# Kernel optimization log

Measured on AMD Instinct MI355X. Metric: run time of the kernel, lower is better.

Reference implementation:

```python
import jax, jax.numpy as jnp
import numpy as np

B, C, H, W = 4, 256, 64, 64
CQ = C // 8


def setup_inputs() -> dict:
    key = jax.random.key(0)
    ks = jax.random.split(key, 8)
    s = 0.02
    return {
        "x": jax.random.normal(ks[0], (B, C, H, W), dtype=jnp.float32),
        "Wq": jax.random.normal(ks[1], (CQ, C), dtype=jnp.float32) * s,
        "bq": jax.random.normal(ks[2], (CQ,), dtype=jnp.float32) * s,
        "Wk": jax.random.normal(ks[3], (CQ, C), dtype=jnp.float32) * s,
        "bk": jax.random.normal(ks[4], (CQ,), dtype=jnp.float32) * s,
        "Wv": jax.random.normal(ks[5], (C, C), dtype=jnp.float32) * s,
        "bv": jax.random.normal(ks[6], (C,), dtype=jnp.float32) * s,
        "gamma": jax.random.normal(ks[7], (1,), dtype=jnp.float32) * s,
    }


def reference(x, Wq, bq, Wk, bk, Wv, bv, gamma):
    b, c, h, w = x.shape
    n = h * w
    xf = x.reshape(b, c, n)  # [B,C,N]; 1x1 conv == channel matmul
    q = jnp.einsum("oc,bcn->bno", Wq, xf) + bq  # [B,N,CQ]
    k = jnp.einsum("oc,bcn->bon", Wk, xf) + bk[:, None]  # [B,CQ,N]
    v = jnp.einsum("oc,bcn->bno", Wv, xf) + bv  # [B,N,C]
    attn = jnp.einsum("bnd,bdm->bnm", q, k)  # [B,N,N], unscaled
    attn = jax.nn.softmax(attn, axis=1)  # non-standard axis (over rows)
    out = jnp.einsum("bnm,bmc->bnc", attn, v)  # [B,N,C]
    out = out.transpose(0, 2, 1).reshape(b, c, h, w)
    return gamma * out + x
```

## Files before the change

kernel.cpp:

```cpp
#include <hip/hip_runtime.h>

#define B_ 4
#define C_ 256
#define N_ 4096
#define LOG2E 1.44269504088896340736f

typedef __attribute__((ext_vector_type(8))) short bf16x8;
typedef __attribute__((ext_vector_type(4))) float f32x4;

static __device__ __forceinline__ unsigned short f2bf(float f) {
    unsigned u = __builtin_bit_cast(unsigned, f);
    u += 0x7fffu + ((u >> 16) & 1u);
    return (unsigned short)(u >> 16);
}

static __device__ __forceinline__ float fexp2(float x) {
#if __has_builtin(__builtin_amdgcn_exp2f)
    return __builtin_amdgcn_exp2f(x);
#else
    return exp2f(x);
#endif
}

#define AS1 __attribute__((address_space(1)))
#define AS3 __attribute__((address_space(3)))
static __device__ __forceinline__ void gload_lds16(const void* g, void* l) {
    __builtin_amdgcn_global_load_lds((const AS1 unsigned*)g, (AS3 unsigned*)l, 16, 0, 0);
}

__global__ void k0_wprep(const float* __restrict__ Wq, const float* __restrict__ Wk,
                         const float* __restrict__ Wv, float* __restrict__ WqkT,
                         float* __restrict__ WvT) {
    int t = blockIdx.x * 256 + threadIdx.x;
    if (t < 256 * 64) {
        int c = t >> 6, o = t & 63;
        WqkT[t] = (o < 32) ? Wq[o * C_ + c] * LOG2E : Wk[(o - 32) * C_ + c];
    }
    int t2 = t - 256 * 64;
    if (t2 >= 0 && t2 < 256 * 256) {
        int cp = t2 >> 8, c = t2 & 255;
        WvT[t2] = Wv[c * C_ + cp];
    }
}

__global__ __launch_bounds__(256) void k1_qk(const float* __restrict__ x,
        const float* __restrict__ WqkT, const float* __restrict__ bq,
        const float* __restrict__ bk, unsigned short* __restrict__ qb,
        unsigned short* __restrict__ ktb) {
    __shared__ float red[4][64][33];
    int b = blockIdx.z, isk = blockIdx.y;
    int l = threadIdx.x & 63, v = threadIdx.x >> 6;
    int n = blockIdx.x * 64 + l;
    float acc[32];
#pragma unroll
    for (int o = 0; o < 32; ++o) acc[o] = 0.0f;
    const float* xp = x + (size_t)b * C_ * N_ + n;
    const float* wbase = WqkT + (isk ? 32 : 0);
#pragma unroll 4
    for (int c = 64 * v; c < 64 * v + 64; ++c) {
        float xv = xp[(size_t)c * N_];
        const float* wr = wbase + c * 64;
#pragma unroll
        for (int o = 0; o < 32; ++o) acc[o] += wr[o] * xv;
    }
#pragma unroll
    for (int o = 0; o < 32; ++o) red[v][l][o] = acc[o];
    __syncthreads();
    int nl = threadIdx.x & 63, ob = (threadIdx.x >> 6) * 8;
    const float* bias = isk ? bk : bq;
    float bs = isk ? 1.0f : LOG2E;
    unsigned pk[4];
#pragma unroll
    for (int i = 0; i < 4; ++i) {
        int o0 = ob + 2 * i, o1 = ob + 2 * i + 1;
        float v0 = red[0][nl][o0] + red[1][nl][o0] + red[2][nl][o0] + red[3][nl][o0] + bias[o0] * bs;
        float v1 = red[0][nl][o1] + red[1][nl][o1] + red[2][nl][o1] + red[3][nl][o1] + bias[o1] * bs;
        pk[i] = (unsigned)f2bf(v0) | ((unsigned)f2bf(v1) << 16);
    }
    unsigned short* dst = (isk ? ktb : qb) + ((size_t)b * N_ + blockIdx.x * 64 + nl) * 32 + ob;
    *(uint4*)dst = make_uint4(pk[0], pk[1], pk[2], pk[3]);
}

__global__ __launch_bounds__(512) void k2_stats(const unsigned short* __restrict__ qb,
        const unsigned short* __restrict__ ktb, float* __restrict__ Wcol) {
    __shared__ float red[64][33];
    int b = blockIdx.y;
    int m0 = blockIdx.x * 64;
    int lane = threadIdx.x & 63, w = threadIdx.x >> 6;
    int r16 = lane & 15, g = lane >> 4;
    const unsigned short* kb = ktb + ((size_t)b * N_ + m0 + r16) * 32 + 8 * g;
    bf16x8 kf0 = *(const bf16x8*)(kb);
    bf16x8 kf1 = *(const bf16x8*)(kb + 16 * 32);
    bf16x8 kf2 = *(const bf16x8*)(kb + 32 * 32);
    bf16x8 kf3 = *(const bf16x8*)(kb + 48 * 32);
    float z0 = 0, z1 = 0, z2 = 0, z3 = 0;
    const unsigned short* qbase = qb + ((size_t)b * N_ + w * 512 + r16) * 32 + 8 * g;
#pragma unroll 2
    for (int n0 = 0; n0 < 512; n0 += 16) {
        bf16x8 qf = *(const bf16x8*)(qbase + (size_t)n0 * 32);
        f32x4 d0 = __builtin_amdgcn_mfma_f32_16x16x32_bf16(qf, kf0, (f32x4){0, 0, 0, 0}, 0, 0, 0);
        f32x4 d1 = __builtin_amdgcn_mfma_f32_16x16x32_bf16(qf, kf1, (f32x4){0, 0, 0, 0}, 0, 0, 0);
        f32x4 d2 = __builtin_amdgcn_mfma_f32_16x16x32_bf16(qf, kf2, (f32x4){0, 0, 0, 0}, 0, 0, 0);
        f32x4 d3 = __builtin_amdgcn_mfma_f32_16x16x32_bf16(qf, kf3, (f32x4){0, 0, 0, 0}, 0, 0, 0);
        z0 += fexp2(d0[0]) + fexp2(d0[1]) + fexp2(d0[2]) + fexp2(d0[3]);
        z1 += fexp2(d1[0]) + fexp2(d1[1]) + fexp2(d1[2]) + fexp2(d1[3]);
        z2 += fexp2(d2[0]) + fexp2(d2[1]) + fexp2(d2[2]) + fexp2(d2[3]);
        z3 += fexp2(d3[0]) + fexp2(d3[1]) + fexp2(d3[2]) + fexp2(d3[3]);
    }
    red[r16][4 * w + g] = z0;
    red[16 + r16][4 * w + g] = z1;
    red[32 + r16][4 * w + g] = z2;
    red[48 + r16][4 * w + g] = z3;
    __syncthreads();
    if (threadIdx.x < 64) {
        float s = 0;
#pragma unroll
        for (int i = 0; i < 32; ++i) s += red[threadIdx.x][i];
        Wcol[(size_t)b * N_ + m0 + threadIdx.x] = 1.0f / s;
    }
}

__global__ __launch_bounds__(256) void k3_v(const float* __restrict__ x,
        const float* __restrict__ WvT, const float* __restrict__ bv,
        const float* __restrict__ Wcol, unsigned short* __restrict__ vtb) {
    int b = blockIdx.z;
    int c0 = blockIdx.y * 32;
    int m = blockIdx.x * 256 + threadIdx.x;
    const float* xp = x + (size_t)b * C_ * N_ + m;
    float acc[32];
#pragma unroll
    for (int j = 0; j < 32; ++j) acc[j] = bv[c0 + j];
#pragma unroll 4
    for (int cp = 0; cp < C_; ++cp) {
        float xv = xp[(size_t)cp * N_];
        const float* wr = WvT + cp * C_ + c0;
#pragma unroll
        for (int j = 0; j < 32; ++j) acc[j] += wr[j] * xv;
    }
    float wm = Wcol[(size_t)b * N_ + m];
#pragma unroll
    for (int j = 0; j < 32; ++j)
        vtb[((size_t)b * C_ + c0 + j) * N_ + m] = f2bf(acc[j] * wm);
}

__global__ __launch_bounds__(512) void k4_pv(const float* __restrict__ x,
        const unsigned short* __restrict__ qb, const unsigned short* __restrict__ ktb,
        const unsigned short* __restrict__ vtb,
        const float* __restrict__ gamma, float* __restrict__ out) {
    __shared__ unsigned short Vl[2][256 * 64];
    __shared__ unsigned short Pl[64 * 64];
    int b = blockIdx.y;
    int n0 = blockIdx.x * 64;
    int lane = threadIdx.x & 63, w = threadIdx.x >> 6;
    int wn = w & 1, wc = w >> 1;
    int r16 = lane & 15, g = lane >> 4;

    const unsigned short* qbp = qb + ((size_t)b * N_ + n0 + 32 * wn + r16) * 32 + 8 * g;
    bf16x8 qf0 = *(const bf16x8*)(qbp);
    bf16x8 qf1 = *(const bf16x8*)(qbp + 16 * 32);

    const unsigned short* kbp = ktb + ((size_t)b * N_ + 16 * wc + r16) * 32 + 8 * g;

    int sc_lo = lane >> 3;
    int s_src = (lane & 7) ^ sc_lo;
    const unsigned short* vsrc = vtb + ((size_t)b * C_ + 32 * w + sc_lo) * N_ + 8 * s_src;

    f32x4 acc[2][4];
#pragma unroll
    for (int i = 0; i < 2; ++i)
#pragma unroll
        for (int j = 0; j < 4; ++j) acc[i][j] = (f32x4){0, 0, 0, 0};

#pragma unroll
    for (int i = 0; i < 4; ++i)
        gload_lds16(vsrc + (size_t)(8 * i) * N_, (char*)&Vl[0][0] + (32 * w + 8 * i) * 128);
    bf16x8 ka = *(const bf16x8*)(kbp);
    __syncthreads();

    int pwb = 32 * wc + 8 * g;
    char* pw0 = (char*)Pl + (32 * wn + r16) * 128 + (pwb ^ ((r16 & 7) << 4));
    char* pw1 = (char*)Pl + (32 * wn + 16 + r16) * 128 + (pwb ^ ((r16 & 7) << 4));

    for (int t = 0; t < 64; ++t) {
        int m0 = t * 64;
        int buf = t & 1;
        f32x4 s0 = __builtin_amdgcn_mfma_f32_16x16x32_bf16(ka, qf0, (f32x4){0, 0, 0, 0}, 0, 0, 0);
        f32x4 s1 = __builtin_amdgcn_mfma_f32_16x16x32_bf16(ka, qf1, (f32x4){0, 0, 0, 0}, 0, 0, 0);
        unsigned a0 = (unsigned)f2bf(fexp2(s0[0])) | ((unsigned)f2bf(fexp2(s0[1])) << 16);
        unsigned a1 = (unsigned)f2bf(fexp2(s0[2])) | ((unsigned)f2bf(fexp2(s0[3])) << 16);
        unsigned a2 = (unsigned)f2bf(fexp2(s1[0])) | ((unsigned)f2bf(fexp2(s1[1])) << 16);
        unsigned a3 = (unsigned)f2bf(fexp2(s1[2])) | ((unsigned)f2bf(fexp2(s1[3])) << 16);
        *(uint2*)pw0 = make_uint2(a0, a1);
        *(uint2*)pw1 = make_uint2(a2, a3);
        __syncthreads();
        if (t < 63) {
            const unsigned short* vs = vsrc + (size_t)(m0 + 64);
#pragma unroll
            for (int i = 0; i < 4; ++i)
                gload_lds16(vs + (size_t)(8 * i) * N_,
                            (char*)&Vl[buf ^ 1][0] + (32 * w + 8 * i) * 128);
            ka = *(const bf16x8*)(kbp + (size_t)(m0 + 64) * 32);
        }
        bf16x8 pa[2][2], vb[4][2];
#pragma unroll
        for (int ns = 0; ns < 2; ++ns) {
            int prow = 32 * wn + 16 * ns + r16;
#pragma unroll
            for (int ks = 0; ks < 2; ++ks)
                pa[ns][ks] = *(const bf16x8*)((char*)Pl + prow * 128 +
                                              ((64 * ks + 16 * g) ^ ((prow & 7) << 4)));
        }
#pragma unroll
        for (int cs = 0; cs < 4; ++cs) {
            int crow = 64 * wc + 16 * cs + r16;
#pragma unroll
            for (int ks = 0; ks < 2; ++ks)
                vb[cs][ks] = *(const bf16x8*)((char*)&Vl[buf][0] + crow * 128 +
                                              ((64 * ks + 16 * g) ^ ((crow & 7) << 4)));
        }
#pragma unroll
        for (int ns = 0; ns < 2; ++ns)
#pragma unroll
            for (int cs = 0; cs < 4; ++cs)
#pragma unroll
                for (int ks = 0; ks < 2; ++ks)
                    acc[ns][cs] = __builtin_amdgcn_mfma_f32_16x16x32_bf16(
                        pa[ns][ks], vb[cs][ks], acc[ns][cs], 0, 0, 0);
        __syncthreads();
    }

    float gm = gamma[0];
#pragma unroll
    for (int ns = 0; ns < 2; ++ns)
#pragma unroll
        for (int cs = 0; cs < 4; ++cs) {
            size_t c = 64 * wc + 16 * cs + r16;
            size_t n = (size_t)n0 + 32 * wn + 16 * ns + 4 * g;
            size_t idx = ((size_t)b * C_ + c) * N_ + n;
            float4 xv = *(const float4*)(x + idx);
            float4 o;
            o.x = gm * acc[ns][cs][0] + xv.x;
            o.y = gm * acc[ns][cs][1] + xv.y;
            o.z = gm * acc[ns][cs][2] + xv.z;
            o.w = gm * acc[ns][cs][3] + xv.w;
            *(float4*)(out + idx) = o;
        }
}

extern "C" void kernel_launch(void* const* d_in, const int* in_sizes, int n_in,
                              void* d_out, int out_size, void* d_ws, size_t ws_size,
                              hipStream_t stream) {
    const float* x = (const float*)d_in[0];
    const float* Wq = (const float*)d_in[1];
    const float* bq = (const float*)d_in[2];
    const float* Wk = (const float*)d_in[3];
    const float* bk = (const float*)d_in[4];
    const float* Wv = (const float*)d_in[5];
    const float* bv = (const float*)d_in[6];
    const float* gamma = (const float*)d_in[7];
    float* out = (float*)d_out;

    char* ws = (char*)d_ws;
    unsigned short* qb  = (unsigned short*)(ws);
    unsigned short* ktb = (unsigned short*)(ws + (1u << 20));
    unsigned short* vtb = (unsigned short*)(ws + (2u << 20));
    float* Wcol = (float*)(ws + (10u << 20));
    float* WqkT = (float*)(ws + (10u << 20) + (1u << 16));
    float* WvT  = (float*)(ws + (10u << 20) + (2u << 16));

    k0_wprep<<<320, 256, 0, stream>>>(Wq, Wk, Wv, WqkT, WvT);
    k1_qk<<<dim3(N_ / 64, 2, B_), 256, 0, stream>>>(x, WqkT, bq, bk, qb, ktb);
    k2_stats<<<dim3(N_ / 64, B_), 512, 0, stream>>>(qb, ktb, Wcol);
    k3_v<<<dim3(N_ / 256, C_ / 32, B_), 256, 0, stream>>>(x, WvT, bv, Wcol, vtb);
    k4_pv<<<dim3(N_ / 64, B_), 512, 0, stream>>>(x, qb, ktb, vtb, gamma, out);
}
```

Measured before the change: 242.1 us.

## Load V directly into registers and double-buffer P in attention kernel

The PV kernel no longer stages V through LDS with global_load_lds. Each wave now owns 32 channels and loads its V fragments straight into registers, prefetching the next tile. P is double-buffered in LDS, and the next tile's QK MFMA and exp are computed after the current PV MFMAs, so only one barrier per iteration remains. The projection kernels also switch their weight reads to float4. This removes LDS traffic and a barrier, at the cost of higher register pressure and more redundant global V reads across blocks.

```diff
diff --git a/kernel.cpp b/kernel.cpp
--- a/kernel.cpp
+++ b/kernel.cpp
@@ -20,12 +20,6 @@
 #else
     return exp2f(x);
 #endif
-}
-
-#define AS1 __attribute__((address_space(1)))
-#define AS3 __attribute__((address_space(3)))
-static __device__ __forceinline__ void gload_lds16(const void* g, void* l) {
-    __builtin_amdgcn_global_load_lds((const AS1 unsigned*)g, (AS3 unsigned*)l, 16, 0, 0);
 }
 
 __global__ void k0_wprep(const float* __restrict__ Wq, const float* __restrict__ Wk,
@@ -59,9 +53,15 @@
 #pragma unroll 4
     for (int c = 64 * v; c < 64 * v + 64; ++c) {
         float xv = xp[(size_t)c * N_];
-        const float* wr = wbase + c * 64;
-#pragma unroll
-        for (int o = 0; o < 32; ++o) acc[o] += wr[o] * xv;
+        const float4* wr4 = (const float4*)(wbase + c * 64);
+#pragma unroll
+        for (int o4 = 0; o4 < 8; ++o4) {
+            float4 wv = wr4[o4];
+            acc[4 * o4 + 0] += wv.x * xv;
+            acc[4 * o4 + 1] += wv.y * xv;
+            acc[4 * o4 + 2] += wv.z * xv;
+            acc[4 * o4 + 3] += wv.w * xv;
+        }
     }
 #pragma unroll
     for (int o = 0; o < 32; ++o) red[v][l][o] = acc[o];
@@ -133,9 +133,15 @@
 #pragma unroll 4
     for (int cp = 0; cp < C_; ++cp) {
         float xv = xp[(size_t)cp * N_];
-        const float* wr = WvT + cp * C_ + c0;
-#pragma unroll
-        for (int j = 0; j < 32; ++j) acc[j] += wr[j] * xv;
+        const float4* wr4 = (const float4*)(WvT + cp * C_ + c0);
+#pragma unroll
+        for (int j4 = 0; j4 < 8; ++j4) {
+            float4 wv = wr4[j4];
+            acc[4 * j4 + 0] += wv.x * xv;
+            acc[4 * j4 + 1] += wv.y * xv;
+            acc[4 * j4 + 2] += wv.z * xv;
+            acc[4 * j4 + 3] += wv.w * xv;
+        }
     }
     float wm = Wcol[(size_t)b * N_ + m];
 #pragma unroll
@@ -147,96 +153,101 @@
         const unsigned short* __restrict__ qb, const unsigned short* __restrict__ ktb,
         const unsigned short* __restrict__ vtb,
         const float* __restrict__ gamma, float* __restrict__ out) {
-    __shared__ unsigned short Vl[2][256 * 64];
-    __shared__ unsigned short Pl[64 * 64];
+    __shared__ unsigned short Pl[2][64 * 64];
     int b = blockIdx.y;
     int n0 = blockIdx.x * 64;
     int lane = threadIdx.x & 63, w = threadIdx.x >> 6;
-    int wn = w & 1, wc = w >> 1;
+    int ms = w >> 1, wn = w & 1;
     int r16 = lane & 15, g = lane >> 4;
+    int swz = (r16 & 7) << 4;
 
     const unsigned short* qbp = qb + ((size_t)b * N_ + n0 + 32 * wn + r16) * 32 + 8 * g;
     bf16x8 qf0 = *(const bf16x8*)(qbp);
     bf16x8 qf1 = *(const bf16x8*)(qbp + 16 * 32);
-
-    const unsigned short* kbp = ktb + ((size_t)b * N_ + 16 * wc + r16) * 32 + 8 * g;
-
-    int sc_lo = lane >> 3;
-    int s_src = (lane & 7) ^ sc_lo;
-    const unsigned short* vsrc = vtb + ((size_t)b * C_ + 32 * w + sc_lo) * N_ + 8 * s_src;
-
-    f32x4 acc[2][4];
-#pragma unroll
-    for (int i = 0; i < 2; ++i)
-#pragma unroll
-        for (int j = 0; j < 4; ++j) acc[i][j] = (f32x4){0, 0, 0, 0};
-
+    const unsigned short* kbp = ktb + ((size_t)b * N_ + 16 * ms + r16) * 32 + 8 * g;
+    const unsigned short* vbp = vtb + ((size_t)b * C_ + 32 * w + r16) * N_ + 8 * g;
+
+    char* pwbase = (char*)&Pl[0][0] + (32 * wn + r16) * 128 + ((32 * ms + 8 * g) ^ swz);
+
+    f32x4 acc[4][2];
 #pragma unroll
     for (int i = 0; i < 4; ++i)
-        gload_lds16(vsrc + (size_t)(8 * i) * N_, (char*)&Vl[0][0] + (32 * w + 8 * i) * 128);
+#pragma unroll
+        for (int j = 0; j < 2; ++j) acc[i][j] = (f32x4){0, 0, 0, 0};
+
     bf16x8 ka = *(const bf16x8*)(kbp);
-    __syncthreads();
-
-    int pwb = 32 * wc + 8 * g;
-    char* pw0 = (char*)Pl + (32 * wn + r16) * 128 + (pwb ^ ((r16 & 7) << 4));
-    char* pw1 = (char*)Pl + (32 * wn + 16 + r16) * 128 + (pwb ^ ((r16 & 7) << 4));
-
-    for (int t = 0; t < 64; ++t) {
-        int m0 = t * 64;
-        int buf = t & 1;
+    bf16x8 vb[2][2], vbn[2][2];
+#pragma unroll
+    for (int cs = 0; cs < 2; ++cs)
+#pragma unroll
+        for (int ks = 0; ks < 2; ++ks)
+            vb[cs][ks] = *(const bf16x8*)(vbp + (size_t)cs * 16 * N_ + 32 * ks);
+    {
         f32x4 s0 = __builtin_amdgcn_mfma_f32_16x16x32_bf16(ka, qf0, (f32x4){0, 0, 0, 0}, 0, 0, 0);
         f32x4 s1 = __builtin_amdgcn_mfma_f32_16x16x32_bf16(ka, qf1, (f32x4){0, 0, 0, 0}, 0, 0, 0);
         unsigned a0 = (unsigned)f2bf(fexp2(s0[0])) | ((unsigned)f2bf(fexp2(s0[1])) << 16);
         unsigned a1 = (unsigned)f2bf(fexp2(s0[2])) | ((unsigned)f2bf(fexp2(s0[3])) << 16);
         unsigned a2 = (unsigned)f2bf(fexp2(s1[0])) | ((unsigned)f2bf(fexp2(s1[1])) << 16);
         unsigned a3 = (unsigned)f2bf(fexp2(s1[2])) | ((unsigned)f2bf(fexp2(s1[3])) << 16);
-        *(uint2*)pw0 = make_uint2(a0, a1);
-        *(uint2*)pw1 = make_uint2(a2, a3);
-        __syncthreads();
+        *(uint2*)(pwbase) = make_uint2(a0, a1);
+        *(uint2*)(pwbase + 16 * 128) = make_uint2(a2, a3);
+    }
+    __syncthreads();
+
+#pragma unroll 2
+    for (int t = 0; t < 64; ++t) {
+        int cbuf = t & 1;
+        bf16x8 kan = ka;
         if (t < 63) {
-            const unsigned short* vs = vsrc + (size_t)(m0 + 64);
-#pragma unroll
-            for (int i = 0; i < 4; ++i)
-                gload_lds16(vs + (size_t)(8 * i) * N_,
-                            (char*)&Vl[buf ^ 1][0] + (32 * w + 8 * i) * 128);
-            ka = *(const bf16x8*)(kbp + (size_t)(m0 + 64) * 32);
-        }
-        bf16x8 pa[2][2], vb[4][2];
-#pragma unroll
-        for (int ns = 0; ns < 2; ++ns) {
-            int prow = 32 * wn + 16 * ns + r16;
+            size_t m1 = (size_t)(t + 1) * 64;
+            kan = *(const bf16x8*)(kbp + m1 * 32);
+#pragma unroll
+            for (int cs = 0; cs < 2; ++cs)
+#pragma unroll
+                for (int ks = 0; ks < 2; ++ks)
+                    vbn[cs][ks] = *(const bf16x8*)(vbp + (size_t)cs * 16 * N_ + m1 + 32 * ks);
+        }
+        const char* prd = (const char*)&Pl[cbuf][0] + r16 * 128;
+        bf16x8 pa[4][2];
+#pragma unroll
+        for (int ns = 0; ns < 4; ++ns)
 #pragma unroll
             for (int ks = 0; ks < 2; ++ks)
-                pa[ns][ks] = *(const bf16x8*)((char*)Pl + prow * 128 +
-                                              ((64 * ks + 16 * g) ^ ((prow & 7) << 4)));
-        }
-#pragma unroll
-        for (int cs = 0; cs < 4; ++cs) {
-            int crow = 64 * wc + 16 * cs + r16;
-#pragma unroll
-            for (int ks = 0; ks < 2; ++ks)
-                vb[cs][ks] = *(const bf16x8*)((char*)&Vl[buf][0] + crow * 128 +
-                                              ((64 * ks + 16 * g) ^ ((crow & 7) << 4)));
-        }
-#pragma unroll
-        for (int ns = 0; ns < 2; ++ns)
-#pragma unroll
-            for (int cs = 0; cs < 4; ++cs)
+                pa[ns][ks] = *(const bf16x8*)(prd + ns * 16 * 128 + ((64 * ks + 16 * g) ^ swz));
+#pragma unroll
+        for (int ns = 0; ns < 4; ++ns)
+#pragma unroll
+            for (int cs = 0; cs < 2; ++cs)
 #pragma unroll
                 for (int ks = 0; ks < 2; ++ks)
                     acc[ns][cs] = __builtin_amdgcn_mfma_f32_16x16x32_bf16(
                         pa[ns][ks], vb[cs][ks], acc[ns][cs], 0, 0, 0);
+        if (t < 63) {
+            f32x4 s0 = __builtin_amdgcn_mfma_f32_16x16x32_bf16(kan, qf0, (f32x4){0, 0, 0, 0}, 0, 0, 0);
+            f32x4 s1 = __builtin_amdgcn_mfma_f32_16x16x32_bf16(kan, qf1, (f32x4){0, 0, 0, 0}, 0, 0, 0);
+            unsigned a0 = (unsigned)f2bf(fexp2(s0[0])) | ((unsigned)f2bf(fexp2(s0[1])) << 16);
+            unsigned a1 = (unsigned)f2bf(fexp2(s0[2])) | ((unsigned)f2bf(fexp2(s0[3])) << 16);
+            unsigned a2 = (unsigned)f2bf(fexp2(s1[0])) | ((unsigned)f2bf(fexp2(s1[1])) << 16);
+            unsigned a3 = (unsigned)f2bf(fexp2(s1[2])) | ((unsigned)f2bf(fexp2(s1[3])) << 16);
+            char* pw = pwbase + (cbuf ^ 1) * 8192;
+            *(uint2*)(pw) = make_uint2(a0, a1);
+            *(uint2*)(pw + 16 * 128) = make_uint2(a2, a3);
+        }
         __syncthreads();
+        ka = kan;
+#pragma unroll
+        for (int cs = 0; cs < 2; ++cs)
+#pragma unroll
+            for (int ks = 0; ks < 2; ++ks) vb[cs][ks] = vbn[cs][ks];
     }
 
     float gm = gamma[0];
 #pragma unroll
-    for (int ns = 0; ns < 2; ++ns)
-#pragma unroll
-        for (int cs = 0; cs < 4; ++cs) {
-            size_t c = 64 * wc + 16 * cs + r16;
-            size_t n = (size_t)n0 + 32 * wn + 16 * ns + 4 * g;
-            size_t idx = ((size_t)b * C_ + c) * N_ + n;
+    for (int ns = 0; ns < 4; ++ns)
+#pragma unroll
+        for (int cs = 0; cs < 2; ++cs) {
+            size_t c = 32 * w + 16 * cs + r16;
+            size_t idx = ((size_t)b * C_ + c) * N_ + n0 + 16 * ns + 4 * g;
             float4 xv = *(const float4*)(x + idx);
             float4 o;
             o.x = gm * acc[ns][cs][0] + xv.x;
```

After: 252.5 us. +4.3%, slower.
